# Performance work log

Measured on AMD Instinct MI355X. Metric: run time of the kernel, lower is better.

Reference implementation:

```python
import jax, jax.numpy as jnp
import numpy as np

B, T, D, H = 4, 4096, 1024, 64

def setup_inputs() -> dict:
    key = jax.random.key(0)
    k1, k2, k3, k4 = jax.random.split(key, 4)
    scale = 1.0 / np.sqrt(D)
    return {
        "x": jax.random.normal(k1, (B, T, D), dtype=jnp.float32),
        "Wq": jax.random.normal(k2, (D, H), dtype=jnp.float32) * scale,
        "Wk": jax.random.normal(k3, (D, H), dtype=jnp.float32) * scale,
        "Wv": jax.random.normal(k4, (D, H), dtype=jnp.float32) * scale,
    }

def reference(x, Wq, Wk, Wv):
    # Projections (Linear without bias): [B,T,H]
    q = jnp.einsum('btd,dh->bth', x, Wq)
    k = jnp.einsum('btd,dh->bth', x, Wk)
    v = jnp.einsum('btd,dh->bth', x, Wv)
    head_size = q.shape[-1]
    # Full T x T scores, scaled by sqrt(head_size) as in the source
    attn = jnp.einsum('bqh,bkh->bqk', q, k) / jnp.sqrt(jnp.float32(head_size))
    t = x.shape[1]
    causal = jnp.tril(jnp.ones((t, t), dtype=bool))  # [T,T]
    attn = jnp.where(causal[None, :, :], attn, -jnp.inf)
    attn = jax.nn.softmax(attn, axis=-1)
    # dropout prob = 0.0 -> identity
    out = jnp.einsum('bqk,bkh->bqh', attn, v)
    return out
```

## Files before the change

### kernel.cpp

```cpp
#include <hip/hip_runtime.h>
#include <hip/hip_bf16.h>
#include <math.h>

#define BB 4
#define TT 4096
#define DD 1024
#define HH 64
#define MTOT (BB * TT)
#define LD 72
#define NCH 4

typedef short short8 __attribute__((ext_vector_type(8)));
typedef float f32x4  __attribute__((ext_vector_type(4)));

__device__ __forceinline__ unsigned short f2bf(float f) {
    unsigned u = __builtin_bit_cast(unsigned, f);
    unsigned r = (u + 0x7fffu + ((u >> 16) & 1u)) >> 16;
    return (unsigned short)r;
}

__device__ __forceinline__ unsigned long long pack4(float a, float b, float c, float d) {
    return (unsigned long long)f2bf(a) |
           ((unsigned long long)f2bf(b) << 16) |
           ((unsigned long long)f2bf(c) << 32) |
           ((unsigned long long)f2bf(d) << 48);
}

__device__ __forceinline__ short8 pack8(float4 a, float4 b) {
    short8 r;
    r[0] = (short)f2bf(a.x); r[1] = (short)f2bf(a.y);
    r[2] = (short)f2bf(a.z); r[3] = (short)f2bf(a.w);
    r[4] = (short)f2bf(b.x); r[5] = (short)f2bf(b.y);
    r[6] = (short)f2bf(b.z); r[7] = (short)f2bf(b.w);
    return r;
}

#define QOFF  0
#define KOFF  (MTOT * HH)
#define VOFF  (2 * MTOT * HH)
#define BF_TOTAL (3 * MTOT * HH)

__global__ __launch_bounds__(256) void transpose_w(
    const float* __restrict__ Wq, const float* __restrict__ Wk,
    const float* __restrict__ Wv, unsigned short* __restrict__ Wt)
{
    const int w = blockIdx.y;
    const float* W = (w == 0) ? Wq : (w == 1) ? Wk : Wv;
    unsigned short* o = Wt + (size_t)w * 64 * 1024;
    const int t  = threadIdx.x;
    const int n4 = t & 15;
    const int k0 = blockIdx.x * 64 + (t >> 4) * 4;

    float v[4][4];
#pragma unroll
    for (int ii = 0; ii < 4; ++ii) {
        float4 r = *(const float4*)&W[(size_t)(k0 + ii) * HH + n4 * 4];
        v[ii][0] = r.x; v[ii][1] = r.y; v[ii][2] = r.z; v[ii][3] = r.w;
    }
#pragma unroll
    for (int cc = 0; cc < 4; ++cc) {
        unsigned long long pk = pack4(v[0][cc], v[1][cc], v[2][cc], v[3][cc]);
        *(unsigned long long*)&o[(size_t)(n4 * 4 + cc) * 1024 + k0] = pk;
    }
}

__global__ __launch_bounds__(256) void qkv_proj(
    const float* __restrict__ x,
    const unsigned short* __restrict__ Wt,
    unsigned short* __restrict__ qkv)
{
    const int tid   = threadIdx.x;
    const int lane  = tid & 63;
    const int wave  = tid >> 6;
    const int l15   = lane & 15;
    const int quad  = lane >> 4;
    const int m0    = blockIdx.x * 32;
    const int strip = wave >> 1;
    const int gh    = wave & 1;

    __shared__ float          Af[32 * 68];
    __shared__ unsigned short Bs[192 * 72];

    f32x4 acc[6];
#pragma unroll
    for (int j = 0; j < 6; ++j) acc[j] = (f32x4){0.f, 0.f, 0.f, 0.f};

    const int arow0 = tid >> 4;
    const int aseg  = tid & 15;
    const int bseg  = tid & 7;

    for (int c = 0; c < 16; ++c) {
        const int kc = c * 64;

#pragma unroll
        for (int i = 0; i < 2; ++i) {
            int row = arow0 + i * 16;
            float4 v = *(const float4*)&x[(size_t)(m0 + row) * DD + kc + aseg * 4];
            *(float4*)&Af[row * 68 + aseg * 4] = v;
        }
#pragma unroll
        for (int i = 0; i < 6; ++i) {
            int tau  = tid + i * 256;
            int gcol = tau >> 3;
            short8 v = *(const short8*)&Wt[(size_t)(gcol >> 6) * 65536 +
                                           (size_t)(gcol & 63) * 1024 + kc + bseg * 8];
            *(short8*)&Bs[gcol * 72 + bseg * 8] = v;
        }
        __syncthreads();

#pragma unroll
        for (int ks = 0; ks < 2; ++ks) {
            const float* ap = &Af[(strip * 16 + l15) * 68 + ks * 32 + quad * 8];
            float4 a0 = *(const float4*)ap;
            float4 a1 = *(const float4*)(ap + 4);
            short8 af = pack8(a0, a1);
#pragma unroll
            for (int j = 0; j < 6; ++j) {
                int g = gh * 6 + j;
                short8 bf = *(const short8*)&Bs[(g * 16 + l15) * 72 + ks * 32 + quad * 8];
                acc[j] = __builtin_amdgcn_mfma_f32_16x16x32_bf16(af, bf, acc[j], 0, 0, 0);
            }
        }
        __syncthreads();
    }

    unsigned short* q_bf  = qkv + QOFF;
    unsigned short* k_bf  = qkv + KOFF;
    unsigned short* vt_bf = qkv + VOFF;
#pragma unroll
    for (int j = 0; j < 6; ++j) {
        int g = gh * 6 + j, w = g >> 2, col = (g & 3) * 16 + l15;
#pragma unroll
        for (int r = 0; r < 4; ++r) {
            int m = m0 + strip * 16 + quad * 4 + r;
            unsigned short bv = f2bf(acc[j][r]);
            if (w == 0)      q_bf[(size_t)m * HH + col] = bv;
            else if (w == 1) k_bf[(size_t)m * HH + col] = bv;
            else {
                int b = m >> 12, t = m & 4095;
                vt_bf[(size_t)b * HH * TT + (size_t)col * TT + t] = bv;
            }
        }
    }
}

__global__ __launch_bounds__(256) void flash_attn(
    const unsigned short* __restrict__ qkv,
    float* __restrict__ Opart,
    float* __restrict__ Mpart,
    float* __restrict__ Lpart)
{
    const int qt = 63 - blockIdx.x;
    const int b  = blockIdx.y;
    const int c  = blockIdx.z;
    if (c * 16 > qt) return;
    const int j0   = c * 16;
    const int jmax = min(j0 + 16, qt + 1);

    const int tid  = threadIdx.x;
    const int lane = tid & 63;
    const int wave = tid >> 6;
    const int l15  = lane & 15;
    const int quad = lane >> 4;

    const unsigned short* q_g  = qkv + QOFF + (size_t)b * TT * HH;
    const unsigned short* k_g  = qkv + KOFF + (size_t)b * TT * HH;
    const unsigned short* vt_g = qkv + VOFF + (size_t)b * HH * TT;

    __shared__ unsigned short Ks[128 * LD];
    __shared__ unsigned short Vs[64 * 136];
    __shared__ unsigned short Ps[4 * 16 * LD];
    unsigned short* Pw = Ps + wave * 16 * LD;

    short8 qf[2];
#pragma unroll
    for (int kk = 0; kk < 2; ++kk)
        qf[kk] = *(const short8*)&q_g[(size_t)(qt * 64 + wave * 16 + l15) * HH + kk * 32 + quad * 8];

    f32x4 ov[4];
#pragma unroll
    for (int i = 0; i < 4; ++i) ov[i] = (f32x4){0.f, 0.f, 0.f, 0.f};
    float m_run = -1e30f, l_run = 0.f;

    const int srow = tid >> 3;
    const int seg  = tid & 7;

    const float SC = 0.125f * 1.44269504088896f;

    for (int jr = j0; jr < jmax; jr += 2) {
        const int nrow = min(jmax - jr, 2) * 64;
        __syncthreads();

#pragma unroll
        for (int r4 = 0; r4 < 4; ++r4) {
            int row = srow + r4 * 32;
            if (row < nrow)
                *(ulonglong2*)&Ks[row * LD + seg * 8] =
                    *(const ulonglong2*)&k_g[(size_t)(jr * 64 + row) * HH + seg * 8];
        }
#pragma unroll
        for (int c2 = 0; c2 < 2; ++c2) {
            int chunk = seg + c2 * 8;
            if (chunk * 8 < nrow) {
#pragma unroll
                for (int r2 = 0; r2 < 2; ++r2) {
                    int h = srow + r2 * 32;
                    *(ulonglong2*)&Vs[h * 136 + chunk * 8] =
                        *(const ulonglong2*)&vt_g[(size_t)h * TT + jr * 64 + chunk * 8];
                }
            }
        }
        __syncthreads();

        const int jend = min(jr + 2, jmax);
        for (int j = jr; j < jend; ++j) {
            const int tl = (j - jr) * 64;

            f32x4 st[4];
#pragma unroll
            for (int i = 0; i < 4; ++i) st[i] = (f32x4){0.f, 0.f, 0.f, 0.f};
#pragma unroll
            for (int kk = 0; kk < 2; ++kk)
#pragma unroll
                for (int mt = 0; mt < 4; ++mt) {
                    short8 a = *(const short8*)&Ks[(tl + mt * 16 + l15) * LD + kk * 32 + quad * 8];
                    st[mt] = __builtin_amdgcn_mfma_f32_16x16x32_bf16(a, qf[kk], st[mt], 0, 0, 0);
                }

#pragma unroll
            for (int mt = 0; mt < 4; ++mt)
#pragma unroll
                for (int r = 0; r < 4; ++r) st[mt][r] *= SC;
            if (j == qt) {
                int qg = wave * 16 + l15;
#pragma unroll
                for (int mt = 0; mt < 4; ++mt)
#pragma unroll
                    for (int r = 0; r < 4; ++r)
                        if (mt * 16 + quad * 4 + r > qg) st[mt][r] = -1e30f;
            }

            float mloc = -1e30f;
#pragma unroll
            for (int mt = 0; mt < 4; ++mt)
#pragma unroll
                for (int r = 0; r < 4; ++r) mloc = fmaxf(mloc, st[mt][r]);
            mloc = fmaxf(mloc, __shfl_xor(mloc, 16));
            mloc = fmaxf(mloc, __shfl_xor(mloc, 32));
            float m_new = fmaxf(m_run, mloc);
            float alpha = exp2f(m_run - m_new);
            m_run = m_new;

            float ssum = 0.f;
#pragma unroll
            for (int mt = 0; mt < 4; ++mt)
#pragma unroll
                for (int r = 0; r < 4; ++r) {
                    float p = exp2f(st[mt][r] - m_new);
                    st[mt][r] = p;
                    ssum += p;
                }
            ssum += __shfl_xor(ssum, 16);
            ssum += __shfl_xor(ssum, 32);
            l_run = l_run * alpha + ssum;

#pragma unroll
            for (int mt = 0; mt < 4; ++mt)
                *(unsigned long long*)&Pw[l15 * LD + mt * 16 + quad * 4] =
                    pack4(st[mt][0], st[mt][1], st[mt][2], st[mt][3]);

            float a4[4];
#pragma unroll
            for (int r = 0; r < 4; ++r) a4[r] = __shfl(alpha, quad * 4 + r);
#pragma unroll
            for (int ht = 0; ht < 4; ++ht)
#pragma unroll
                for (int r = 0; r < 4; ++r) ov[ht][r] *= a4[r];

#pragma unroll
            for (int kk = 0; kk < 2; ++kk) {
                short8 a = *(const short8*)&Pw[l15 * LD + kk * 32 + quad * 8];
#pragma unroll
                for (int ht = 0; ht < 4; ++ht) {
                    short8 bf = *(const short8*)&Vs[(ht * 16 + l15) * 136 + tl + kk * 32 + quad * 8];
                    ov[ht] = __builtin_amdgcn_mfma_f32_16x16x32_bf16(a, bf, ov[ht], 0, 0, 0);
                }
            }
        }
    }

    float* Ob = Opart + ((size_t)((b * 64 + qt) * NCH + c)) * 4096;
#pragma unroll
    for (int ht = 0; ht < 4; ++ht)
#pragma unroll
        for (int r = 0; r < 4; ++r)
            Ob[(size_t)(wave * 16 + quad * 4 + r) * HH + ht * 16 + l15] = ov[ht][r];
    if (quad == 0) {
        size_t mi = (size_t)((b * 64 + qt) * NCH + c) * 64 + wave * 16 + l15;
        Mpart[mi] = m_run;
        Lpart[mi] = l_run;
    }
}

__global__ __launch_bounds__(256) void combine(
    const float* __restrict__ Opart,
    const float* __restrict__ Mpart,
    const float* __restrict__ Lpart,
    float* __restrict__ out)
{
    const int qt = blockIdx.x;
    const int b  = blockIdx.y;
    const int nc = (qt >> 4) + 1;
    const int t  = threadIdx.x;
    const int row = t >> 2;
    const int seg = t & 3;

    const size_t base = (size_t)(b * 64 + qt) * NCH;

    float m_c[NCH], M = -1e30f;
    for (int c = 0; c < nc; ++c) {
        m_c[c] = Mpart[(base + c) * 64 + row];
        M = fmaxf(M, m_c[c]);
    }
    float L = 0.f, w_c[NCH];
    for (int c = 0; c < nc; ++c) {
        w_c[c] = exp2f(m_c[c] - M);
        L += w_c[c] * Lpart[(base + c) * 64 + row];
    }
    float invL = 1.0f / L;

    f32x4 o[4];
#pragma unroll
    for (int i = 0; i < 4; ++i) o[i] = (f32x4){0.f, 0.f, 0.f, 0.f};
    for (int c = 0; c < nc; ++c) {
        const float* Ob = Opart + (base + c) * 4096 + (size_t)row * HH + seg * 16;
#pragma unroll
        for (int i = 0; i < 4; ++i) {
            f32x4 v = *(const f32x4*)(Ob + i * 4);
            o[i] += v * w_c[c];
        }
    }
    float* op = out + ((size_t)b * TT + qt * 64 + row) * HH + seg * 16;
#pragma unroll
    for (int i = 0; i < 4; ++i)
        *(f32x4*)(op + i * 4) = o[i] * invL;
}

extern "C" void kernel_launch(void* const* d_in, const int* in_sizes, int n_in,
                              void* d_out, int out_size, void* d_ws, size_t ws_size,
                              hipStream_t stream) {
    const float* x  = (const float*)d_in[0];
    const float* Wq = (const float*)d_in[1];
    const float* Wk = (const float*)d_in[2];
    const float* Wv = (const float*)d_in[3];
    float* out = (float*)d_out;

    unsigned short* qkv = (unsigned short*)d_ws;
    float* Opart = (float*)((char*)d_ws + BF_TOTAL * 2);
    float* Mpart = Opart + (size_t)BB * 64 * NCH * 4096;
    float* Lpart = Mpart + (size_t)BB * 64 * NCH * 64;

    unsigned short* Wt = (unsigned short*)d_out;

    transpose_w<<<dim3(16, 3), 256, 0, stream>>>(Wq, Wk, Wv, Wt);
    qkv_proj<<<dim3(MTOT / 32), 256, 0, stream>>>(x, Wt, qkv);
    flash_attn<<<dim3(64, BB, NCH), 256, 0, stream>>>(qkv, Opart, Mpart, Lpart);
    combine<<<dim3(64, BB), 256, 0, stream>>>(Opart, Mpart, Lpart, out);
}
```

Baseline: 189.5 us.

## Double-buffer QKV projection tiles with direct global-to-LDS loads and XOR swizzle

```diff
diff --git a/kernel.cpp b/kernel.cpp
--- a/kernel.cpp
+++ b/kernel.cpp
@@ -12,6 +12,7 @@
 
 typedef short short8 __attribute__((ext_vector_type(8)));
 typedef float f32x4  __attribute__((ext_vector_type(4)));
+typedef unsigned int u32;
 
 __device__ __forceinline__ unsigned short f2bf(float f) {
     unsigned u = __builtin_bit_cast(unsigned, f);
@@ -33,6 +34,12 @@
     r[4] = (short)f2bf(b.x); r[5] = (short)f2bf(b.y);
     r[6] = (short)f2bf(b.z); r[7] = (short)f2bf(b.w);
     return r;
+}
+
+__device__ __forceinline__ void gl16(const void* g, void* l) {
+    __builtin_amdgcn_global_load_lds(
+        (const __attribute__((address_space(1))) u32*)g,
+        (__attribute__((address_space(3))) u32*)l, 16, 0, 0);
 }
 
 #define QOFF  0
@@ -64,7 +71,7 @@
     }
 }
 
-__global__ __launch_bounds__(256) void qkv_proj(
+__global__ __launch_bounds__(256, 2) void qkv_proj(
     const float* __restrict__ x,
     const unsigned short* __restrict__ Wt,
     unsigned short* __restrict__ qkv)
@@ -75,65 +82,78 @@
     const int l15   = lane & 15;
     const int quad  = lane >> 4;
     const int m0    = blockIdx.x * 32;
-    const int strip = wave >> 1;
-    const int gh    = wave & 1;
-
-    __shared__ float          Af[32 * 68];
-    __shared__ unsigned short Bs[192 * 72];
+    const int strip = wave & 1;
+    const int half  = wave >> 1;
+
+    __shared__ float          Af[2][32 * 64];
+    __shared__ unsigned short Bs[2][192 * 64];
+
+    const int ar  = lane >> 4;
+    const int as  = lane & 15;
+    const int bc  = lane >> 3;
+    const int bs2 = (lane & 7) ^ bc;
+
+#define STAGE(it, p)                                                         \
+    {                                                                        \
+        const int kc_ = (it) * 64;                                           \
+        _Pragma("unroll")                                                    \
+        for (int jj = 0; jj < 2; ++jj) {                                     \
+            int j   = wave * 2 + jj;                                         \
+            int row = 4 * j + ar;                                            \
+            int sw  = as ^ (row & 15);                                       \
+            gl16(x + (size_t)(m0 + row) * DD + kc_ + sw * 4,                 \
+                 &Af[p][j * 256]);                                           \
+        }                                                                    \
+        _Pragma("unroll")                                                    \
+        for (int jj = 0; jj < 6; ++jj) {                                     \
+            int j    = wave * 6 + jj;                                        \
+            int gcol = 8 * j + bc;                                           \
+            gl16(Wt + (size_t)gcol * 1024 + kc_ + bs2 * 8,                   \
+                 &Bs[p][j * 512]);                                           \
+        }                                                                    \
+    }
 
     f32x4 acc[6];
 #pragma unroll
-    for (int j = 0; j < 6; ++j) acc[j] = (f32x4){0.f, 0.f, 0.f, 0.f};
-
-    const int arow0 = tid >> 4;
-    const int aseg  = tid & 15;
-    const int bseg  = tid & 7;
-
-    for (int c = 0; c < 16; ++c) {
-        const int kc = c * 64;
-
-#pragma unroll
-        for (int i = 0; i < 2; ++i) {
-            int row = arow0 + i * 16;
-            float4 v = *(const float4*)&x[(size_t)(m0 + row) * DD + kc + aseg * 4];
-            *(float4*)&Af[row * 68 + aseg * 4] = v;
-        }
-#pragma unroll
-        for (int i = 0; i < 6; ++i) {
-            int tau  = tid + i * 256;
-            int gcol = tau >> 3;
-            short8 v = *(const short8*)&Wt[(size_t)(gcol >> 6) * 65536 +
-                                           (size_t)(gcol & 63) * 1024 + kc + bseg * 8];
-            *(short8*)&Bs[gcol * 72 + bseg * 8] = v;
+    for (int i = 0; i < 6; ++i) acc[i] = (f32x4){0.f, 0.f, 0.f, 0.f};
+
+    STAGE(0, 0)
+    __syncthreads();
+    int p = 0;
+
+    for (int it = 0; it < 16; ++it) {
+        if (it < 15) STAGE(it + 1, p ^ 1)
+
+        const int row = strip * 16 + l15;
+#pragma unroll
+        for (int ks = 0; ks < 2; ++ks) {
+            int c0 = ks * 8 + quad * 2;
+            float4 a0 = *(const float4*)&Af[p][row * 64 + ((c0)     ^ l15) * 4];
+            float4 a1 = *(const float4*)&Af[p][row * 64 + ((c0 + 1) ^ l15) * 4];
+            short8 af = pack8(a0, a1);
+            int cb = (ks * 4 + quad) ^ (l15 & 7);
+#pragma unroll
+            for (int jj = 0; jj < 6; ++jj) {
+                int col = (half * 6 + jj) * 16 + l15;
+                short8 bfr = *(const short8*)&Bs[p][col * 64 + cb * 8];
+                acc[jj] = __builtin_amdgcn_mfma_f32_16x16x32_bf16(af, bfr, acc[jj], 0, 0, 0);
+            }
         }
         __syncthreads();
-
-#pragma unroll
-        for (int ks = 0; ks < 2; ++ks) {
-            const float* ap = &Af[(strip * 16 + l15) * 68 + ks * 32 + quad * 8];
-            float4 a0 = *(const float4*)ap;
-            float4 a1 = *(const float4*)(ap + 4);
-            short8 af = pack8(a0, a1);
-#pragma unroll
-            for (int j = 0; j < 6; ++j) {
-                int g = gh * 6 + j;
-                short8 bf = *(const short8*)&Bs[(g * 16 + l15) * 72 + ks * 32 + quad * 8];
-                acc[j] = __builtin_amdgcn_mfma_f32_16x16x32_bf16(af, bf, acc[j], 0, 0, 0);
-            }
-        }
-        __syncthreads();
-    }
+        p ^= 1;
+    }
+#undef STAGE
 
     unsigned short* q_bf  = qkv + QOFF;
     unsigned short* k_bf  = qkv + KOFF;
     unsigned short* vt_bf = qkv + VOFF;
 #pragma unroll
-    for (int j = 0; j < 6; ++j) {
-        int g = gh * 6 + j, w = g >> 2, col = (g & 3) * 16 + l15;
+    for (int jj = 0; jj < 6; ++jj) {
+        int g = half * 6 + jj, w = g >> 2, col = (g & 3) * 16 + l15;
 #pragma unroll
         for (int r = 0; r < 4; ++r) {
             int m = m0 + strip * 16 + quad * 4 + r;
-            unsigned short bv = f2bf(acc[j][r]);
+            unsigned short bv = f2bf(acc[jj][r]);
             if (w == 0)      q_bf[(size_t)m * HH + col] = bv;
             else if (w == 1) k_bf[(size_t)m * HH + col] = bv;
             else {
```

Measured after the change: 167.8 us. 1.13x faster.
